# Kernel optimization log

Measured on AMD Instinct MI355X. Metric: run time of the kernel, lower is better.

Reference implementation:

```python
import jax, jax.numpy as jnp
import numpy as np

N_DIM = 768
HIDDEN_DIM = 768
BATCH = 4
SEQ = 2048


def setup_inputs() -> dict:
    key = jax.random.key(0)
    ks = jax.random.split(key, 9)
    s_in = 1.0 / np.sqrt(N_DIM)
    s_h = 1.0 / np.sqrt(HIDDEN_DIM)
    return {
        "x": jax.random.normal(ks[0], (BATCH, SEQ, N_DIM), dtype=jnp.float32),
        # torch Linear weights: [out_features, in_features]
        "wq": jax.random.uniform(ks[1], (HIDDEN_DIM, N_DIM), jnp.float32, -s_in, s_in),
        "bq": jax.random.uniform(ks[2], (HIDDEN_DIM,), jnp.float32, -s_in, s_in),
        "wk": jax.random.uniform(ks[3], (HIDDEN_DIM, N_DIM), jnp.float32, -s_in, s_in),
        "bk": jax.random.uniform(ks[4], (HIDDEN_DIM,), jnp.float32, -s_in, s_in),
        "wv": jax.random.uniform(ks[5], (HIDDEN_DIM, N_DIM), jnp.float32, -s_in, s_in),
        "bv": jax.random.uniform(ks[6], (HIDDEN_DIM,), jnp.float32, -s_in, s_in),
        "wo": jax.random.uniform(ks[7], (N_DIM, HIDDEN_DIM), jnp.float32, -s_h, s_h),
        "bo": jax.random.uniform(ks[8], (N_DIM,), jnp.float32, -s_h, s_h),
    }


def reference(x, wq, bq, wk, bk, wv, bv, wo, bo):
    # q,k,v: [B, S, H]
    q = jnp.einsum("bsd,hd->bsh", x, wq) + bq
    k = jnp.einsum("bsd,hd->bsh", x, wk) + bk
    v = jnp.einsum("bsd,hd->bsh", x, wv) + bv
    # NOTE: faithful to source — no 1/sqrt(d) scaling, no mask.
    scores = jnp.einsum("bqh,bkh->bqk", q, k)  # [B, S, S]
    attn = jax.nn.softmax(scores, axis=-1)
    y = jnp.einsum("bqk,bkh->bqh", attn, v)  # [B, S, H]
    out = jnp.einsum("bsh,dh->bsd", y, wo) + bo
    return out
```

## Files before the change

### kernel.cpp

```cpp
#include <hip/hip_runtime.h>

typedef _Float16 f16;
typedef _Float16 f16x8 __attribute__((ext_vector_type(8)));
typedef float f32x4 __attribute__((ext_vector_type(4)));

#define GLD16(g, l) __builtin_amdgcn_global_load_lds( \
    (const __attribute__((address_space(1))) void*)(g), \
    (__attribute__((address_space(3))) void*)(l), 16, 0, 0)

template <typename OutT, int BM, int BN, int MODE, int MINW>
__global__ __launch_bounds__(256, MINW)
void gemm_kernel(const f16* __restrict__ A, long sA,
                 const f16* __restrict__ B, long sB,
                 void* __restrict__ Cv, long sC,
                 void* __restrict__ C2v,
                 const float* __restrict__ bias,
                 const float* __restrict__ bias2,
                 int N, int K)
{
    constexpr int FM = BM / 32;
    constexpr int FN = BN / 32;
    constexpr int IA = BM / 32;
    constexpr int IB = BN / 32;

    OutT* C  = (OutT*)Cv;
    OutT* C2 = (OutT*)C2v;
    const int tid  = threadIdx.x;
    const int wave = tid >> 6;
    const int lane = tid & 63;
    const int bz   = blockIdx.z;
    A += (long)bz * sA;
    B += (long)bz * sB;
    C += (long)bz * sC;
    const long bm = (long)blockIdx.x * BM;
    const long bn = (long)blockIdx.y * BN;

    __shared__ f16 sAt[BM * 64];
    __shared__ f16 sBt[BN * 64];

    const int srow = lane >> 3;
    const int gch  = ((lane & 7) ^ srow) * 8;

    const f16* gAb = A + (bm + wave * (BM / 4) + srow) * (long)K + gch;
    const f16* gBb = B + (bn + wave * (BN / 4) + srow) * (long)K + gch;

    const int wm = (wave >> 1) * (BM / 2);
    const int wn = (wave & 1) * (BN / 2);
    const int lr = lane & 15;
    const int qd = lane >> 4;
    const int swz0 = ((0 * 4 + qd) ^ (lr & 7)) * 8;
    const int swz1 = ((1 * 4 + qd) ^ (lr & 7)) * 8;

    f32x4 acc[FM][FN] = {};

    for (int k0 = 0; k0 < K; k0 += 64) {
        #pragma unroll
        for (int i = 0; i < IA; ++i)
            GLD16(gAb + k0 + (long)i * 8 * K, &sAt[(wave * (BM / 4) + i * 8) * 64]);
        #pragma unroll
        for (int i = 0; i < IB; ++i)
            GLD16(gBb + k0 + (long)i * 8 * K, &sBt[(wave * (BN / 4) + i * 8) * 64]);
        __syncthreads();

        #pragma unroll
        for (int h = 0; h < 2; ++h) {
            const int swz = h ? swz1 : swz0;
            f16x8 af[FM], bf[FN];
            #pragma unroll
            for (int t = 0; t < FM; ++t)
                af[t] = *(const f16x8*)&sAt[(wm + t * 16 + lr) * 64 + swz];
            #pragma unroll
            for (int t = 0; t < FN; ++t)
                bf[t] = *(const f16x8*)&sBt[(wn + t * 16 + lr) * 64 + swz];
            #pragma unroll
            for (int tm = 0; tm < FM; ++tm)
                #pragma unroll
                for (int tn = 0; tn < FN; ++tn)
                    acc[tm][tn] = __builtin_amdgcn_mfma_f32_16x16x32_f16(
                        af[tm], bf[tn], acc[tm][tn], 0, 0, 0);
        }
        __syncthreads();
    }

    #pragma unroll
    for (int tn = 0; tn < FN; ++tn) {
        const long col = bn + wn + tn * 16 + lr;
        OutT* dst = C;
        long cc = col, stride = N;
        float bc = 0.f;
        if (MODE == 1) bc = bias[col];
        if (MODE == 3) {
            stride = 768;
            if (col >= 768) { dst = C2; cc = col - 768; bc = bias2[cc]; }
            else            { bc = bias[cc]; }
        }
        #pragma unroll
        for (int tm = 0; tm < FM; ++tm) {
            #pragma unroll
            for (int r = 0; r < 4; ++r) {
                const long row = bm + wm + tm * 16 + qd * 4 + r;
                float v = acc[tm][tn][r] + bc;
                if (MODE == 2) v += bias[row];
                dst[row * stride + cc] = (OutT)v;
            }
        }
    }
}

__global__ __launch_bounds__(512, 2)
void gemm_pipe(const f16* __restrict__ A, long sA,
               const f16* __restrict__ B, long sB,
               f16* __restrict__ C, long sC,
               int N, int K)
{
    const int tid  = threadIdx.x;
    const int wave = tid >> 6;
    const int lane = tid & 63;
    const int bz   = blockIdx.z;
    A += (long)bz * sA;
    B += (long)bz * sB;
    C += (long)bz * sC;
    const long bm = (long)blockIdx.x * 256;
    const long bn = (long)blockIdx.y * 256;

    __shared__ f16 sAt[2][256 * 64];
    __shared__ f16 sBt[2][256 * 64];

    const int srow = lane >> 3;
    const int gch  = ((lane & 7) ^ srow) * 8;
    const f16* gA = A + (bm + wave * 32 + srow) * (long)K + gch;
    const f16* gB = B + (bn + wave * 32 + srow) * (long)K + gch;

    const int wm = (wave >> 2) * 128;
    const int wn = (wave & 3) * 64;
    const int lr = lane & 15;
    const int qd = lane >> 4;
    const int swz0 = ((0 * 4 + qd) ^ (lr & 7)) * 8;
    const int swz1 = ((1 * 4 + qd) ^ (lr & 7)) * 8;

    f32x4 acc[8][4] = {};

    #pragma unroll
    for (int i = 0; i < 4; ++i)
        GLD16(gA + (long)i * 8 * K, &sAt[0][(wave * 32 + i * 8) * 64]);
    #pragma unroll
    for (int i = 0; i < 4; ++i)
        GLD16(gB + (long)i * 8 * K, &sBt[0][(wave * 32 + i * 8) * 64]);
    __syncthreads();

    const int nt = K / 64;
    for (int t = 0; t < nt; ++t) {
        const int cur = t & 1;
        if (t + 1 < nt) {
            const long off = (long)(t + 1) * 64;
            #pragma unroll
            for (int i = 0; i < 4; ++i)
                GLD16(gA + off + (long)i * 8 * K, &sAt[cur ^ 1][(wave * 32 + i * 8) * 64]);
            #pragma unroll
            for (int i = 0; i < 4; ++i)
                GLD16(gB + off + (long)i * 8 * K, &sBt[cur ^ 1][(wave * 32 + i * 8) * 64]);
        }
        #pragma unroll
        for (int h = 0; h < 2; ++h) {
            const int swz = h ? swz1 : swz0;
            f16x8 bf[4];
            #pragma unroll
            for (int c = 0; c < 4; ++c)
                bf[c] = *(const f16x8*)&sBt[cur][(wn + c * 16 + lr) * 64 + swz];
            #pragma unroll
            for (int rh = 0; rh < 2; ++rh) {
                f16x8 af[4];
                #pragma unroll
                for (int m = 0; m < 4; ++m)
                    af[m] = *(const f16x8*)&sAt[cur][(wm + rh * 64 + m * 16 + lr) * 64 + swz];
                __builtin_amdgcn_s_setprio(1);
                #pragma unroll
                for (int m = 0; m < 4; ++m)
                    #pragma unroll
                    for (int c = 0; c < 4; ++c)
                        acc[rh * 4 + m][c] = __builtin_amdgcn_mfma_f32_16x16x32_f16(
                            af[m], bf[c], acc[rh * 4 + m][c], 0, 0, 0);
                __builtin_amdgcn_s_setprio(0);
            }
        }
        __syncthreads();
    }

    #pragma unroll
    for (int cf = 0; cf < 4; ++cf) {
        const long col = bn + wn + cf * 16 + lr;
        #pragma unroll
        for (int rf = 0; rf < 8; ++rf) {
            #pragma unroll
            for (int r = 0; r < 4; ++r) {
                const long row = bm + wm + rf * 16 + qd * 4 + r;
                C[row * (long)N + col] = (f16)acc[rf][cf][r];
            }
        }
    }
}

__global__ __launch_bounds__(256)
void softmax_kernel(f16* __restrict__ S)
{
    const long row = blockIdx.x;
    f16* p = S + row * 2048;
    const int tid  = threadIdx.x;
    const int wave = tid >> 6;
    const int lane = tid & 63;

    f16x8 x = *(const f16x8*)&p[tid * 8];
    float v[8];
    float m = -1e30f;
    #pragma unroll
    for (int j = 0; j < 8; ++j) { v[j] = (float)x[j]; m = fmaxf(m, v[j]); }
    #pragma unroll
    for (int off = 32; off > 0; off >>= 1) m = fmaxf(m, __shfl_down(m, off));

    __shared__ float rm[4], rs[4];
    if (lane == 0) rm[wave] = m;
    __syncthreads();
    m = fmaxf(fmaxf(rm[0], rm[1]), fmaxf(rm[2], rm[3]));

    float s = 0.f;
    #pragma unroll
    for (int j = 0; j < 8; ++j) { v[j] = __expf(v[j] - m); s += v[j]; }
    #pragma unroll
    for (int off = 32; off > 0; off >>= 1) s += __shfl_down(s, off);
    if (lane == 0) rs[wave] = s;
    __syncthreads();
    s = rs[0] + rs[1] + rs[2] + rs[3];
    const float inv = 1.0f / s;

    f16x8 y;
    #pragma unroll
    for (int j = 0; j < 8; ++j) y[j] = (f16)(v[j] * inv);
    *(f16x8*)&p[tid * 8] = y;
}

__global__ __launch_bounds__(256)
void cvt_all_kernel(const float* __restrict__ x,
                    const float* __restrict__ w0, const float* __restrict__ w1,
                    const float* __restrict__ w2, const float* __restrict__ w3,
                    f16* __restrict__ x16, f16* __restrict__ w16)
{
    const float* in; f16* out; long i;
    if (blockIdx.x < 3072) {
        in = x; out = x16;
        i = ((long)blockIdx.x * 256 + threadIdx.x) * 8;
    } else {
        const int wb  = blockIdx.x - 3072;
        const int sel = wb / 288;
        in  = (sel == 0) ? w0 : (sel == 1) ? w1 : (sel == 2) ? w2 : w3;
        out = w16 + (long)sel * 589824;
        i = ((long)(wb - sel * 288) * 256 + threadIdx.x) * 8;
    }
    float4 a = *(const float4*)(in + i);
    float4 b = *(const float4*)(in + i + 4);
    f16x8 o;
    o[0] = (f16)a.x; o[1] = (f16)a.y; o[2] = (f16)a.z; o[3] = (f16)a.w;
    o[4] = (f16)b.x; o[5] = (f16)b.y; o[6] = (f16)b.z; o[7] = (f16)b.w;
    *(f16x8*)&out[i] = o;
}

extern "C" void kernel_launch(void* const* d_in, const int* in_sizes, int n_in,
                              void* d_out, int out_size, void* d_ws, size_t ws_size,
                              hipStream_t stream)
{
    const float* x  = (const float*)d_in[0];
    const float* wq = (const float*)d_in[1];
    const float* bq = (const float*)d_in[2];
    const float* wk = (const float*)d_in[3];
    const float* bk = (const float*)d_in[4];
    const float* wv = (const float*)d_in[5];
    const float* bv = (const float*)d_in[6];
    const float* wo = (const float*)d_in[7];
    const float* bo = (const float*)d_in[8];

    char* ws = (char*)d_ws;
    f16* x16 = (f16*)(ws + 0);
    f16* w16 = (f16*)(ws + 12582912);
    f16* Q   = (f16*)(ws + 17301504);
    f16* Kb  = (f16*)(ws + 29884416);
    f16* VT  = (f16*)(ws + 42467328);
    f16* S   = (f16*)(ws + 55050240);
    f16* Y   = (f16*)(ws + 88604672);

    f16* wv16 = w16 + 2 * 589824;
    f16* wo16 = w16 + 3 * 589824;

    cvt_all_kernel<<<4224, 256, 0, stream>>>(x, wq, wk, wv, wo, x16, w16);

    gemm_kernel<f16, 128, 128, 3, 3><<<dim3(64, 12, 1), 256, 0, stream>>>(
        x16, 0, w16, 0, Q, 0, Kb, bq, bk, 1536, 768);
    gemm_kernel<f16, 128, 128, 2, 3><<<dim3(6, 16, 4), 256, 0, stream>>>(
        wv16, 0, x16, (long)2048 * 768, VT, (long)768 * 2048, nullptr,
        bv, nullptr, 2048, 768);
    gemm_pipe<<<dim3(8, 8, 4), 512, 0, stream>>>(
        Q, (long)2048 * 768, Kb, (long)2048 * 768, S, (long)2048 * 2048,
        2048, 768);
    softmax_kernel<<<8192, 256, 0, stream>>>(S);
    gemm_kernel<f16, 128, 128, 0, 3><<<dim3(16, 6, 4), 256, 0, stream>>>(
        S, (long)2048 * 2048, VT, (long)768 * 2048, Y, (long)2048 * 768,
        nullptr, nullptr, nullptr, 768, 2048);
    gemm_kernel<float, 128, 128, 1, 3><<<dim3(64, 6, 1), 256, 0, stream>>>(
        Y, 0, wo16, 0, (float*)d_out, 0, nullptr, bo, nullptr, 768, 768);
}
```

Before: 244.5 us.

## Add double-buffered gemm_pipe4 with explicit vmcnt waits and smaller tiles

Adds a templated gemm_pipe4 kernel that double-buffers async global-to-LDS loads. It waits with an explicit s_waitcnt vmcnt so the prefetch of the next tile stays in flight while the current tile is computed, and uses raw s_barrier in place of __syncthreads. The V projection, attn·V and output projection GEMMs switch to it with 64x128 or 128x64 tiles, which doubles the block count to improve CU fill. gemm_pipe gets the same waitcnt/barrier change and loses its initial sync. The risks are fragile manual waitcnt counting and lower per-block reuse from the smaller tiles.

```diff
diff --git a/kernel.cpp b/kernel.cpp
--- a/kernel.cpp
+++ b/kernel.cpp
@@ -107,6 +107,122 @@
     }
 }
 
+template <typename OutT, int BM, int BN, int MODE, int MINW>
+__global__ __launch_bounds__(256, MINW)
+void gemm_pipe4(const f16* __restrict__ A, long sA,
+                const f16* __restrict__ B, long sB,
+                void* __restrict__ Cv, long sC,
+                void* __restrict__ C2v,
+                const float* __restrict__ bias,
+                const float* __restrict__ bias2,
+                int N, int K)
+{
+    constexpr int FM = BM / 32;
+    constexpr int FN = BN / 32;
+    constexpr int IA = BM / 32;
+    constexpr int IB = BN / 32;
+
+    OutT* C  = (OutT*)Cv;
+    OutT* C2 = (OutT*)C2v;
+    const int tid  = threadIdx.x;
+    const int wave = tid >> 6;
+    const int lane = tid & 63;
+    const int bz   = blockIdx.z;
+    A += (long)bz * sA;
+    B += (long)bz * sB;
+    C += (long)bz * sC;
+    const long bm = (long)blockIdx.x * BM;
+    const long bn = (long)blockIdx.y * BN;
+
+    __shared__ f16 sAt[2][BM * 64];
+    __shared__ f16 sBt[2][BN * 64];
+
+    const int srow = lane >> 3;
+    const int gch  = ((lane & 7) ^ srow) * 8;
+
+    const f16* gAb = A + (bm + wave * (BM / 4) + srow) * (long)K + gch;
+    const f16* gBb = B + (bn + wave * (BN / 4) + srow) * (long)K + gch;
+
+    const int wm = (wave >> 1) * (BM / 2);
+    const int wn = (wave & 1) * (BN / 2);
+    const int lr = lane & 15;
+    const int qd = lane >> 4;
+    const int swz0 = ((0 * 4 + qd) ^ (lr & 7)) * 8;
+    const int swz1 = ((1 * 4 + qd) ^ (lr & 7)) * 8;
+
+    f32x4 acc[FM][FN] = {};
+
+    #pragma unroll
+    for (int i = 0; i < IA; ++i)
+        GLD16(gAb + (long)i * 8 * K, &sAt[0][(wave * (BM / 4) + i * 8) * 64]);
+    #pragma unroll
+    for (int i = 0; i < IB; ++i)
+        GLD16(gBb + (long)i * 8 * K, &sBt[0][(wave * (BN / 4) + i * 8) * 64]);
+
+    const int nt = K / 64;
+    for (int t = 0; t < nt; ++t) {
+        const int cur = t & 1;
+        if (t + 1 < nt) {
+            const long off = (long)(t + 1) * 64;
+            #pragma unroll
+            for (int i = 0; i < IA; ++i)
+                GLD16(gAb + off + (long)i * 8 * K, &sAt[cur ^ 1][(wave * (BM / 4) + i * 8) * 64]);
+            #pragma unroll
+            for (int i = 0; i < IB; ++i)
+                GLD16(gBb + off + (long)i * 8 * K, &sBt[cur ^ 1][(wave * (BN / 4) + i * 8) * 64]);
+            asm volatile("s_waitcnt vmcnt(%0)" :: "n"(IA + IB));
+        } else {
+            asm volatile("s_waitcnt vmcnt(0)");
+        }
+        __builtin_amdgcn_s_barrier();
+
+        #pragma unroll
+        for (int h = 0; h < 2; ++h) {
+            const int swz = h ? swz1 : swz0;
+            f16x8 af[FM], bf[FN];
+            #pragma unroll
+            for (int t2 = 0; t2 < FM; ++t2)
+                af[t2] = *(const f16x8*)&sAt[cur][(wm + t2 * 16 + lr) * 64 + swz];
+            #pragma unroll
+            for (int t2 = 0; t2 < FN; ++t2)
+                bf[t2] = *(const f16x8*)&sBt[cur][(wn + t2 * 16 + lr) * 64 + swz];
+            __builtin_amdgcn_s_setprio(1);
+            #pragma unroll
+            for (int tm = 0; tm < FM; ++tm)
+                #pragma unroll
+                for (int tn = 0; tn < FN; ++tn)
+                    acc[tm][tn] = __builtin_amdgcn_mfma_f32_16x16x32_f16(
+                        af[tm], bf[tn], acc[tm][tn], 0, 0, 0);
+            __builtin_amdgcn_s_setprio(0);
+        }
+        __builtin_amdgcn_s_barrier();
+    }
+
+    #pragma unroll
+    for (int tn = 0; tn < FN; ++tn) {
+        const long col = bn + wn + tn * 16 + lr;
+        OutT* dst = C;
+        long cc = col, stride = N;
+        float bc = 0.f;
+        if (MODE == 1) bc = bias[col];
+        if (MODE == 3) {
+            stride = 768;
+            if (col >= 768) { dst = C2; cc = col - 768; bc = bias2[cc]; }
+            else            { bc = bias[cc]; }
+        }
+        #pragma unroll
+        for (int tm = 0; tm < FM; ++tm) {
+            #pragma unroll
+            for (int r = 0; r < 4; ++r) {
+                const long row = bm + wm + tm * 16 + qd * 4 + r;
+                float v = acc[tm][tn][r] + bc;
+                if (MODE == 2) v += bias[row];
+                dst[row * stride + cc] = (OutT)v;
+            }
+        }
+    }
+}
+
 __global__ __launch_bounds__(512, 2)
 void gemm_pipe(const f16* __restrict__ A, long sA,
                const f16* __restrict__ B, long sB,
@@ -146,7 +262,6 @@
     #pragma unroll
     for (int i = 0; i < 4; ++i)
         GLD16(gB + (long)i * 8 * K, &sBt[0][(wave * 32 + i * 8) * 64]);
-    __syncthreads();
 
     const int nt = K / 64;
     for (int t = 0; t < nt; ++t) {
@@ -159,7 +274,12 @@
             #pragma unroll
             for (int i = 0; i < 4; ++i)
                 GLD16(gB + off + (long)i * 8 * K, &sBt[cur ^ 1][(wave * 32 + i * 8) * 64]);
-        }
+            asm volatile("s_waitcnt vmcnt(8)");
+        } else {
+            asm volatile("s_waitcnt vmcnt(0)");
+        }
+        __builtin_amdgcn_s_barrier();
+
         #pragma unroll
         for (int h = 0; h < 2; ++h) {
             const int swz = h ? swz1 : swz0;
@@ -183,7 +303,7 @@
                 __builtin_amdgcn_s_setprio(0);
             }
         }
-        __syncthreads();
+        __builtin_amdgcn_s_barrier();
     }
 
     #pragma unroll
@@ -293,16 +413,16 @@
 
     gemm_kernel<f16, 128, 128, 3, 3><<<dim3(64, 12, 1), 256, 0, stream>>>(
         x16, 0, w16, 0, Q, 0, Kb, bq, bk, 1536, 768);
-    gemm_kernel<f16, 128, 128, 2, 3><<<dim3(6, 16, 4), 256, 0, stream>>>(
+    gemm_pipe4<f16, 64, 128, 2, 4><<<dim3(12, 16, 4), 256, 0, stream>>>(
         wv16, 0, x16, (long)2048 * 768, VT, (long)768 * 2048, nullptr,
         bv, nullptr, 2048, 768);
     gemm_pipe<<<dim3(8, 8, 4), 512, 0, stream>>>(
         Q, (long)2048 * 768, Kb, (long)2048 * 768, S, (long)2048 * 2048,
         2048, 768);
     softmax_kernel<<<8192, 256, 0, stream>>>(S);
-    gemm_kernel<f16, 128, 128, 0, 3><<<dim3(16, 6, 4), 256, 0, stream>>>(
+    gemm_pipe4<f16, 128, 64, 0, 4><<<dim3(16, 12, 4), 256, 0, stream>>>(
         S, (long)2048 * 2048, VT, (long)768 * 2048, Y, (long)2048 * 768,
         nullptr, nullptr, nullptr, 768, 2048);
-    gemm_kernel<float, 128, 128, 1, 3><<<dim3(64, 6, 1), 256, 0, stream>>>(
+    gemm_pipe4<float, 128, 64, 1, 4><<<dim3(64, 12, 1), 256, 0, stream>>>(
         Y, 0, wo16, 0, (float*)d_out, 0, nullptr, bo, nullptr, 768, 768);
 }
```

Measured after the change: 230.2 us. 1.06x faster.
